# Kernel optimization log

Hardware: AMD Instinct MI355X
Metric: run time of the kernel (lower is better)

The kernel has to match this reference:

```python
import jax, jax.numpy as jnp
import numpy as np
from jax import lax

DN = ('NCHW', 'OIHW', 'NCHW')
NUM_IN_CAPS = 1152  # 32 * 6 * 6
NUM_OUT_CAPS = 10
IN_CAP_DIM = 8
OUT_CAP_DIM = 16
ROUTING_ITERS = 3


def squash(x):
    # unit_v * |x|^2 / (1 + |x|^2), norm over last dim
    n = jnp.linalg.norm(x, axis=-1, keepdims=True)
    return (x / n) * (n * n / (1.0 + n * n))


def setup_inputs() -> dict:
    key = jax.random.key(0)
    ks = jax.random.split(key, 12)
    B = 256
    return {
        'x': jax.random.normal(ks[0], (B, 1, 28, 28), jnp.float32),
        'conv1_w': jax.random.normal(ks[1], (256, 1, 9, 9), jnp.float32) * 0.05,
        'conv1_b': jnp.zeros((256,), jnp.float32),
        'pconv_w': jax.random.normal(ks[2], (256, 256, 9, 9), jnp.float32) * 0.02,
        'pconv_b': jnp.zeros((256,), jnp.float32),
        'W_caps': jax.random.normal(ks[3], (NUM_IN_CAPS, NUM_OUT_CAPS, OUT_CAP_DIM, IN_CAP_DIM), jnp.float32),
        'dec_w1': jax.random.normal(ks[4], (160, 512), jnp.float32) * 0.05,
        'dec_b1': jnp.zeros((512,), jnp.float32),
        'dec_w2': jax.random.normal(ks[5], (512, 1024), jnp.float32) * 0.04,
        'dec_b2': jnp.zeros((1024,), jnp.float32),
        'dec_w3': jax.random.normal(ks[6], (1024, 784), jnp.float32) * 0.03,
        'dec_b3': jnp.zeros((784,), jnp.float32),
    }


def reference(x, conv1_w, conv1_b, pconv_w, pconv_b, W_caps,
              dec_w1, dec_b1, dec_w2, dec_b2, dec_w3, dec_b3):
    # conv1: 1 -> 256, k9, s1, no activation (faithful to source)
    h = lax.conv_general_dilated(x, conv1_w, (1, 1), 'VALID', dimension_numbers=DN)
    h = h + conv1_b[None, :, None, None]  # (B,256,20,20)
    # primary caps conv: 256 -> 32*8, k9, s2
    h = lax.conv_general_dilated(h, pconv_w, (2, 2), 'VALID', dimension_numbers=DN)
    h = h + pconv_b[None, :, None, None]  # (B,256,6,6)
    B = h.shape[0]
    u_in = squash(h.reshape(B, -1, IN_CAP_DIM))  # (B,1152,8)
    # prediction vectors u_hat: (B,1152,10,16)
    u = jnp.einsum('ijab,nib->nija', W_caps, u_in)
    # routing-by-agreement; b is shared across batch and accumulates batch-summed agreement (faithful)
    b = jnp.zeros((NUM_IN_CAPS, NUM_OUT_CAPS), u.dtype)
    v = None
    for r in range(ROUTING_ITERS + 1):
        c = jax.nn.softmax(b, axis=-1)             # (1152,10)
        s = jnp.einsum('ij,nija->nja', c, u)        # (B,10,16)
        v = squash(s)
        if r < ROUTING_ITERS:
            b = b + jnp.einsum('nija,nja->ij', u, v)
    # decoder path: mask by predicted class
    logits = jnp.linalg.norm(v, axis=-1)            # (B,10)
    label = jnp.argmax(logits, axis=1)
    one_hot = jax.nn.one_hot(label, NUM_OUT_CAPS, dtype=v.dtype)
    recon = (one_hot[..., None] * v).reshape(B, NUM_OUT_CAPS * OUT_CAP_DIM)
    recon = jax.nn.relu(recon @ dec_w1 + dec_b1)
    recon = jax.nn.relu(recon @ dec_w2 + dec_b2)
    recon = jax.nn.sigmoid(recon @ dec_w3 + dec_b3)  # (B,784)
    return (v, recon)
```

## Files before the change

### kernel.cpp

```cpp
#include <hip/hip_runtime.h>
#include <hip/hip_fp16.h>
#include <math.h>


typedef __attribute__((ext_vector_type(8))) short short8;
typedef __attribute__((ext_vector_type(4))) float floatx4;

__device__ __forceinline__ unsigned short bf16_rne(float f) {
    unsigned int u = __float_as_uint(f);
    return (unsigned short)((u + 0x7FFFu + ((u >> 16) & 1u)) >> 16);
}
__device__ __forceinline__ float bf16_tof(unsigned short h) {
    return __uint_as_float((unsigned int)h << 16);
}
__device__ __forceinline__ void load_lds16(const void* g, void* l) {
    __builtin_amdgcn_global_load_lds(
        (const __attribute__((address_space(1))) unsigned int*)g,
        (__attribute__((address_space(3))) unsigned int*)l, 16, 0, 0);
}

__global__ __launch_bounds__(256, 2) void conv1_kernel(
    const float* __restrict__ x, const float* __restrict__ w,
    const float* __restrict__ bias, unsigned short* __restrict__ xpack)
{
    __shared__ float xs[784];
    __shared__ float wl[64 * 81];
    int t = threadIdx.x;
    int n = blockIdx.x;
    int cot = blockIdx.y;

    for (int j = t; j < 784; j += 256) xs[j] = x[n * 784 + j];
    {
        int co_s = t >> 2, k0 = (t & 3) * 21;
        const float* wsrc = w + (size_t)(cot * 64 + co_s) * 81;
        #pragma unroll
        for (int k = 0; k < 21; ++k)
            if (k0 + k < 81) wl[co_s * 81 + k0 + k] = wsrc[k0 + k];
    }
    __syncthreads();

    int co_l = t & 63, slot = t >> 6;
    int co = cot * 64 + co_l;
    float bv = bias[co];
    for (int r5 = 0; r5 < 5; ++r5) {
        int py = slot * 5 + r5;
        float acc[20];
        #pragma unroll
        for (int i = 0; i < 20; i++) acc[i] = bv;
        #pragma unroll
        for (int ky = 0; ky < 9; ++ky) {
            float xr[28];
            const float4* rowp = (const float4*)&xs[(py + ky) * 28];
            #pragma unroll
            for (int q = 0; q < 7; q++) {
                float4 v4 = rowp[q];
                xr[4*q] = v4.x; xr[4*q+1] = v4.y; xr[4*q+2] = v4.z; xr[4*q+3] = v4.w;
            }
            #pragma unroll
            for (int kx = 0; kx < 9; ++kx) {
                float wv = wl[co_l * 81 + ky * 9 + kx];
                #pragma unroll
                for (int px = 0; px < 20; ++px) acc[px] += wv * xr[px + kx];
            }
        }
        #pragma unroll
        for (int px = 0; px < 20; ++px) {
            float v = acc[px];
            unsigned short h = bf16_rne(v);
            unsigned short l = bf16_rne(v - bf16_tof(h));
            size_t pix = (size_t)n * 400 + py * 20 + px;
            xpack[pix * 512 + co] = h;
            xpack[pix * 512 + 256 + co] = l;
        }
    }
}

__global__ __launch_bounds__(256) void wpack_kernel(
    const float* __restrict__ w, unsigned short* __restrict__ wp)
{
    int tid = blockIdx.x * 256 + threadIdx.x;
    if (tid >= 648 * 16 * 64) return;
    int lane = tid & 63, g = (tid >> 6) & 15, gs = tid >> 10;
    int cb = gs & 7, kk = gs >> 3;
    int ky = kk / 9, kx = kk - ky * 9;
    int n16 = lane & 15, q = lane >> 4;
    int co = g * 16 + n16;
    unsigned short hi[8], lo[8];
    #pragma unroll
    for (int j = 0; j < 8; ++j) {
        int ci = cb * 32 + q * 8 + j;
        float v = w[((size_t)co * 256 + ci) * 81 + ky * 9 + kx];
        hi[j] = bf16_rne(v);
        lo[j] = bf16_rne(v - bf16_tof(hi[j]));
    }
    unsigned short* dst = wp + ((size_t)gs * 16 + g) * 1024 + lane * 8;
    *(short8*)dst         = *(short8*)hi;
    *(short8*)(dst + 512) = *(short8*)lo;
}

__global__ __launch_bounds__(256, 2) void pconv_mfma_kernel(
    const unsigned short* __restrict__ xp, const unsigned short* __restrict__ wp,
    __half* __restrict__ P3)
{
    __shared__ unsigned char lds[16384];
    int t = threadIdx.x;
    int lane = t & 63;
    int w = __builtin_amdgcn_readfirstlane(t >> 6);
    int mtile = blockIdx.x, kc = blockIdx.y;
    int m16 = lane & 15, q = lane >> 4;

    unsigned int asrc[2];
    #pragma unroll
    for (int j = 0; j < 2; ++j) {
        int r = w * 16 + j * 8 + (lane >> 3);
        int m = mtile * 64 + r;
        int n = m / 36, pos = m - n * 36;
        int oy = pos / 6, ox = pos - oy * 6;
        int pixbase = n * 400 + oy * 40 + ox * 2;
        int pp = (lane & 7) ^ (lane >> 3);
        int partoff = (pp < 4) ? pp * 16 : 512 + (pp - 4) * 16;
        asrc[j] = (unsigned int)(pixbase * 1024 + partoff);
    }
    const char* xb = (const char*)xp;
    const char* wb = (const char*)wp;

    floatx4 acc[4][4];
    #pragma unroll
    for (int a = 0; a < 4; ++a)
        #pragma unroll
        for (int b = 0; b < 4; ++b) acc[a][b] = (floatx4){0.f, 0.f, 0.f, 0.f};

    int slot_hi = (q ^ (m16 & 7)) * 16;
    int slot_lo = slot_hi ^ 64;

    auto stageA = [&](int s, int buf) {
        int gs = kc * 216 + s; if (gs > 647) gs = 647;
        int kk = gs >> 3, cb = gs & 7;
        int ky = kk / 9, kx = kk - ky * 9;
        unsigned int delta = (unsigned int)((ky * 20 + kx) * 1024 + cb * 64);
        #pragma unroll
        for (int j = 0; j < 2; ++j)
            load_lds16(xb + asrc[j] + delta,
                       (void*)(lds + buf * 8192 + w * 2048 + j * 1024));
    };
    auto loadB = [&](int s, short8* Bh, short8* Bl) {
        int gs = kc * 216 + s; if (gs > 647) gs = 647;
        #pragma unroll
        for (int c = 0; c < 4; ++c) {
            const char* bp = wb + ((size_t)gs * 16 + (w * 4 + c)) * 2048 + lane * 16;
            Bh[c] = *(const short8*)bp;
            Bl[c] = *(const short8*)(bp + 1024);
        }
    };
    auto compute = [&](int buf, short8* Bh, short8* Bl) {
        #pragma unroll
        for (int ms = 0; ms < 4; ++ms) {
            const char* base = (const char*)lds + buf * 8192 + (ms * 16 + m16) * 128;
            short8 Ah = *(const short8*)(base + slot_hi);
            short8 Al = *(const short8*)(base + slot_lo);
            #pragma unroll
            for (int c = 0; c < 4; ++c) {
                acc[ms][c] = __builtin_amdgcn_mfma_f32_16x16x32_bf16(Ah, Bh[c], acc[ms][c], 0, 0, 0);
                acc[ms][c] = __builtin_amdgcn_mfma_f32_16x16x32_bf16(Ah, Bl[c], acc[ms][c], 0, 0, 0);
                acc[ms][c] = __builtin_amdgcn_mfma_f32_16x16x32_bf16(Al, Bh[c], acc[ms][c], 0, 0, 0);
            }
        }
    };

    short8 Bh0[4], Bl0[4], Bh1[4], Bl1[4];
    stageA(0, 0);
    loadB(0, Bh0, Bl0);
    __syncthreads();
    for (int s = 0; s < 216; s += 2) {
        stageA(s + 1, 1);
        loadB(s + 1, Bh1, Bl1);
        compute(0, Bh0, Bl0);
        __syncthreads();
        stageA(s + 2, 0);
        loadB(s + 2, Bh0, Bl0);
        compute(1, Bh1, Bl1);
        __syncthreads();
    }

    __half* outp = P3 + ((size_t)kc * 9216 + (size_t)mtile * 64) * 256;
    #pragma unroll
    for (int ms = 0; ms < 4; ++ms)
        #pragma unroll
        for (int r = 0; r < 4; ++r) {
            int ml = ms * 16 + q * 4 + r;
            #pragma unroll
            for (int c = 0; c < 4; ++c) {
                int co = w * 64 + c * 16 + m16;
                outp[ml * 256 + co] = __float2half(acc[ms][c][r]);
            }
        }
}

__global__ __launch_bounds__(256) void squash_u_kernel(
    const __half* __restrict__ P3, const float* __restrict__ pb, float* __restrict__ u)
{
    int cap = blockIdx.x * 256 + threadIdx.x;
    int n = cap / 1152;
    int capl = cap - n * 1152;
    float z[8]; float n2 = 0.f;
    #pragma unroll
    for (int b = 0; b < 8; ++b) {
        int q2 = capl * 8 + b;
        int co = q2 / 36;
        int pos = q2 - co * 36;
        int m = n * 36 + pos;
        float s = 0.f;
        #pragma unroll
        for (int kc = 0; kc < 3; ++kc)
            s += __half2float(P3[((size_t)kc * 9216 + m) * 256 + co]);
        s += pb[co];
        z[b] = s; n2 += s * s;
    }
    float sc = sqrtf(n2) / (1.0f + n2);
    float4* op = (float4*)(u + (size_t)cap * 8);
    op[0] = make_float4(z[0]*sc, z[1]*sc, z[2]*sc, z[3]*sc);
    op[1] = make_float4(z[4]*sc, z[5]*sc, z[6]*sc, z[7]*sc);
}

__global__ void softmax_c_kernel(const float* __restrict__ b, float* __restrict__ c)
{
    int i = blockIdx.x * 256 + threadIdx.x;
    if (i >= 1152) return;
    float e[10], m = -1e30f;
    #pragma unroll
    for (int j = 0; j < 10; j++) { e[j] = b[i * 10 + j]; m = fmaxf(m, e[j]); }
    float sum = 0.f;
    #pragma unroll
    for (int j = 0; j < 10; j++) { e[j] = expf(e[j] - m); sum += e[j]; }
    float inv = 1.f / sum;
    #pragma unroll
    for (int j = 0; j < 10; j++) c[i * 10 + j] = e[j] * inv;
}

__global__ __launch_bounds__(256, 2) void s_kernel(
    const float* __restrict__ c, const float* __restrict__ u,
    const float* __restrict__ W, float* __restrict__ sbuf)
{
    int t = threadIdx.x;
    int a = t & 15, nl = t >> 4;
    int nt = blockIdx.x;
    int bz = blockIdx.y;
    int i0 = bz * 24;
    int n0 = nt * 32 + nl * 2;
    float acc[2][10];
    #pragma unroll
    for (int r = 0; r < 2; ++r)
        #pragma unroll
        for (int j = 0; j < 10; ++j) acc[r][j] = 0.f;

    for (int i = i0; i < i0 + 24; ++i) {
        const float* cb = &c[i * 10];
        float4 u0[2], u1[2];
        #pragma unroll
        for (int r = 0; r < 2; ++r) {
            const float4* up = (const float4*)&u[(size_t)(n0 + r) * 9216 + (size_t)i * 8];
            u0[r] = up[0]; u1[r] = up[1];
        }
        #pragma unroll
        for (int j = 0; j < 10; ++j) {
            const float4* wpt = (const float4*)&W[(((size_t)i * 10 + j) * 16 + a) * 8];
            float4 w0 = wpt[0], w1 = wpt[1];
            float cij = cb[j];
            #pragma unroll
            for (int r = 0; r < 2; ++r) {
                float d = w0.x*u0[r].x + w0.y*u0[r].y + w0.z*u0[r].z + w0.w*u0[r].w
                        + w1.x*u1[r].x + w1.y*u1[r].y + w1.z*u1[r].z + w1.w*u1[r].w;
                acc[r][j] += cij * d;
            }
        }
    }
    #pragma unroll
    for (int r = 0; r < 2; ++r)
        #pragma unroll
        for (int j = 0; j < 10; ++j)
            sbuf[(size_t)bz * 40960 + (((size_t)(n0 + r) * 10 + j) * 16) + a] = acc[r][j];
}

__global__ __launch_bounds__(256) void squash_v_kernel(const float* __restrict__ sbuf,
                                float* __restrict__ v, float* __restrict__ vout)
{
    int t = threadIdx.x;
    int a = t & 15;
    int idx = blockIdx.x * 16 + (t >> 4);
    float s = 0.f;
    #pragma unroll
    for (int z = 0; z < 48; ++z) s += sbuf[(size_t)z * 40960 + idx * 16 + a];
    float n2 = s * s;
    n2 += __shfl_xor(n2, 1);
    n2 += __shfl_xor(n2, 2);
    n2 += __shfl_xor(n2, 4);
    n2 += __shfl_xor(n2, 8);
    float sc = sqrtf(n2) / (1.0f + n2);
    float y = s * sc;
    v[idx * 16 + a] = y;
    if (vout) vout[idx * 16 + a] = y;
}

__global__ __launch_bounds__(192) void bupd_kernel(
    const float* __restrict__ u, const float* __restrict__ v,
    const float* __restrict__ W, float* __restrict__ b)
{
    int i0 = blockIdx.x * 4;
    int n0 = blockIdx.y * 128;
    int t = threadIdx.x;
    if (t >= 160) return;
    int j = t >> 4, a = t & 15;
    float g4[4][8];
    #pragma unroll
    for (int g = 0; g < 4; ++g)
        #pragma unroll
        for (int k = 0; k < 8; ++k) g4[g][k] = 0.f;

    for (int n = n0; n < n0 + 128; ++n) {
        float vv = v[n * 160 + t];
        const float4* ub = (const float4*)&u[(size_t)n * 9216 + (size_t)i0 * 8];
        #pragma unroll
        for (int g = 0; g < 4; ++g) {
            float4 q0 = ub[g * 2], q1 = ub[g * 2 + 1];
            g4[g][0] += q0.x * vv; g4[g][1] += q0.y * vv; g4[g][2] += q0.z * vv; g4[g][3] += q0.w * vv;
            g4[g][4] += q1.x * vv; g4[g][5] += q1.y * vv; g4[g][6] += q1.z * vv; g4[g][7] += q1.w * vv;
        }
    }
    #pragma unroll
    for (int g = 0; g < 4; ++g) {
        int i = i0 + g;
        const float4* wpt = (const float4*)&W[(((size_t)i * 10 + j) * 16 + a) * 8];
        float4 w0 = wpt[0], w1 = wpt[1];
        float p = w0.x*g4[g][0] + w0.y*g4[g][1] + w0.z*g4[g][2] + w0.w*g4[g][3]
                + w1.x*g4[g][4] + w1.y*g4[g][5] + w1.z*g4[g][6] + w1.w*g4[g][7];
        p += __shfl_xor(p, 1);
        p += __shfl_xor(p, 2);
        p += __shfl_xor(p, 4);
        p += __shfl_xor(p, 8);
        if (a == 0) atomicAdd(&b[i * 10 + j], p);
    }
}

__global__ void mask_kernel(const float* __restrict__ v, float* __restrict__ out)
{
    int n = threadIdx.x;
    const float* vp = &v[n * 160];
    int best = 0; float bestv = -1.f;
    for (int j = 0; j < 10; j++) {
        float n2 = 0.f;
        #pragma unroll
        for (int a = 0; a < 16; a++) { float y = vp[j * 16 + a]; n2 += y * y; }
        float ln = sqrtf(n2);
        if (ln > bestv) { bestv = ln; best = j; }
    }
    for (int j = 0; j < 10; j++)
        for (int a = 0; a < 16; a++)
            out[n * 160 + j * 16 + a] = (j == best) ? vp[j * 16 + a] : 0.f;
}

template<int K, int KCH, int O>
__global__ __launch_bounds__(256, 2) void mlp_part_kernel(
    const float* __restrict__ X, const float* __restrict__ Wm,
    float* __restrict__ partial)
{
    __shared__ float XS[KCH * 16];
    int t = threadIdx.x;
    int og = t & 63, ns = t >> 6;
    int n0 = blockIdx.x * 16;
    int o = blockIdx.y * 256 + og * 4;
    int o_c = min(o, O - 4);
    int ks = blockIdx.z;
    int kc0 = ks * KCH;

    for (int idx = t; idx < KCH * 16; idx += 256) {
        int k_l = idx >> 4, n_l = idx & 15;
        XS[k_l * 16 + n_l] = X[(size_t)(n0 + n_l) * K + kc0 + k_l];
    }
    __syncthreads();

    float acc[4][4];
    #pragma unroll
    for (int r = 0; r < 4; ++r)
        #pragma unroll
        for (int q = 0; q < 4; ++q) acc[r][q] = 0.f;

    #pragma unroll 8
    for (int k = 0; k < KCH; ++k) {
        float4 wv = *(const float4*)&Wm[(size_t)(kc0 + k) * O + o_c];
        float4 xs4 = *(const float4*)&XS[k * 16 + ns * 4];
        acc[0][0] += xs4.x * wv.x; acc[0][1] += xs4.x * wv.y; acc[0][2] += xs4.x * wv.z; acc[0][3] += xs4.x * wv.w;
        acc[1][0] += xs4.y * wv.x; acc[1][1] += xs4.y * wv.y; acc[1][2] += xs4.y * wv.z; acc[1][3] += xs4.y * wv.w;
        acc[2][0] += xs4.z * wv.x; acc[2][1] += xs4.z * wv.y; acc[2][2] += xs4.z * wv.z; acc[2][3] += xs4.z * wv.w;
        acc[3][0] += xs4.w * wv.x; acc[3][1] += xs4.w * wv.y; acc[3][2] += xs4.w * wv.z; acc[3][3] += xs4.w * wv.w;
    }

    if (o < O) {
        float* pp = partial + ((size_t)ks * 256 + n0 + ns * 4) * O + o;
        #pragma unroll
        for (int r = 0; r < 4; ++r)
            *(float4*)(pp + (size_t)r * O) = make_float4(acc[r][0], acc[r][1], acc[r][2], acc[r][3]);
    }
}

template<int KS, int O, int ACT>
__global__ __launch_bounds__(256) void mlp_reduce_kernel(
    const float* __restrict__ partial, const float* __restrict__ bias,
    float* __restrict__ out)
{
    int n = blockIdx.y;
    int o = (blockIdx.x * 256 + threadIdx.x) * 4;
    if (o >= O) return;
    float4 s = make_float4(0.f, 0.f, 0.f, 0.f);
    #pragma unroll
    for (int ks = 0; ks < KS; ++ks) {
        float4 p = *(const float4*)&partial[((size_t)ks * 256 + n) * O + o];
        s.x += p.x; s.y += p.y; s.z += p.z; s.w += p.w;
    }
    float4 bv = *(const float4*)&bias[o];
    float r[4] = {s.x + bv.x, s.y + bv.y, s.z + bv.z, s.w + bv.w};
    #pragma unroll
    for (int q = 0; q < 4; ++q)
        r[q] = (ACT == 0) ? fmaxf(r[q], 0.f) : (1.f / (1.f + expf(-r[q])));
    *(float4*)&out[(size_t)n * O + o] = make_float4(r[0], r[1], r[2], r[3]);
}

extern "C" void kernel_launch(void* const* d_in, const int* in_sizes, int n_in,
                              void* d_out, int out_size, void* d_ws, size_t ws_size,
                              hipStream_t stream)
{
    const float* x       = (const float*)d_in[0];
    const float* conv1_w = (const float*)d_in[1];
    const float* conv1_b = (const float*)d_in[2];
    const float* pconv_w = (const float*)d_in[3];
    const float* pconv_b = (const float*)d_in[4];
    const float* W_caps  = (const float*)d_in[5];
    const float* dec_w1  = (const float*)d_in[6];
    const float* dec_b1  = (const float*)d_in[7];
    const float* dec_w2  = (const float*)d_in[8];
    const float* dec_b2  = (const float*)d_in[9];
    const float* dec_w3  = (const float*)d_in[10];
    const float* dec_b3  = (const float*)d_in[11];
    float* out = (float*)d_out;

    float* ws = (float*)d_ws;
    size_t off = 0;
    auto alloc = [&](size_t nf) { float* p = ws + off; off += (nf + 63) & ~(size_t)63; return p; };
    unsigned short* xpack = (unsigned short*)alloc(26214400);
    unsigned short* wpack = (unsigned short*)alloc(5308416);
    __half* P3  = (__half*)alloc(3538944);
    float* u_in = alloc(2359296);
    float* bbuf = alloc(11520);
    float* cbuf = alloc(11520);
    float* sbuf = alloc(48 * 40960);
    float* vbuf = alloc(40960);
    float* rin  = alloc(40960);
    float* mpart = alloc(8 * 256 * 1024);
    float* h1   = alloc(131072);
    float* h2   = alloc(262144);

    hipMemsetAsync(bbuf, 0, 11520 * sizeof(float), stream);

    wpack_kernel<<<(648 * 16 * 64 + 255) / 256, 256, 0, stream>>>(pconv_w, wpack);
    conv1_kernel<<<dim3(256, 4), 256, 0, stream>>>(x, conv1_w, conv1_b, xpack);
    pconv_mfma_kernel<<<dim3(144, 3), 256, 0, stream>>>(xpack, wpack, P3);
    squash_u_kernel<<<1152, 256, 0, stream>>>(P3, pconv_b, u_in);

    for (int r = 0; r < 4; ++r) {
        softmax_c_kernel<<<5, 256, 0, stream>>>(bbuf, cbuf);
        s_kernel<<<dim3(8, 48), 256, 0, stream>>>(cbuf, u_in, W_caps, sbuf);
        squash_v_kernel<<<160, 256, 0, stream>>>(sbuf, vbuf, (r == 3) ? out : nullptr);
        if (r < 3) bupd_kernel<<<dim3(288, 2), 192, 0, stream>>>(u_in, vbuf, W_caps, bbuf);
    }

    mask_kernel<<<1, 256, 0, stream>>>(vbuf, rin);

    mlp_part_kernel<160, 80, 512><<<dim3(16, 2, 2), 256, 0, stream>>>(rin, dec_w1, mpart);
    mlp_reduce_kernel<2, 512, 0><<<dim3(1, 256), 256, 0, stream>>>(mpart, dec_b1, h1);
    mlp_part_kernel<512, 128, 1024><<<dim3(16, 4, 4), 256, 0, stream>>>(h1, dec_w2, mpart);
    mlp_reduce_kernel<4, 1024, 0><<<dim3(1, 256), 256, 0, stream>>>(mpart, dec_b2, h2);
    mlp_part_kernel<1024, 128, 784><<<dim3(16, 4, 8), 256, 0, stream>>>(h2, dec_w3, mpart);
    mlp_reduce_kernel<8, 784, 1><<<dim3(1, 256), 256, 0, stream>>>(mpart, dec_b3, out + 40960);
}
```

Measured before the change: 841.7 us.

## Switch pconv split-precision from bf16x3 to fp16x2, fuse softmax into s_kernel

```diff
diff --git a/kernel.cpp b/kernel.cpp
--- a/kernel.cpp
+++ b/kernel.cpp
@@ -3,15 +3,20 @@
 #include <math.h>
 
 
+typedef __attribute__((ext_vector_type(8))) _Float16 half8;
 typedef __attribute__((ext_vector_type(8))) short short8;
 typedef __attribute__((ext_vector_type(4))) float floatx4;
 
-__device__ __forceinline__ unsigned short bf16_rne(float f) {
-    unsigned int u = __float_as_uint(f);
-    return (unsigned short)((u + 0x7FFFu + ((u >> 16) & 1u)) >> 16);
-}
-__device__ __forceinline__ float bf16_tof(unsigned short h) {
-    return __uint_as_float((unsigned int)h << 16);
+__device__ __forceinline__ unsigned short f16bits(float v) {
+    _Float16 h = (_Float16)v;
+    unsigned short b;
+    __builtin_memcpy(&b, &h, 2);
+    return b;
+}
+__device__ __forceinline__ float f16back(unsigned short b) {
+    _Float16 h;
+    __builtin_memcpy(&h, &b, 2);
+    return (float)h;
 }
 __device__ __forceinline__ void load_lds16(const void* g, void* l) {
     __builtin_amdgcn_global_load_lds(
@@ -66,8 +71,8 @@
         #pragma unroll
         for (int px = 0; px < 20; ++px) {
             float v = acc[px];
-            unsigned short h = bf16_rne(v);
-            unsigned short l = bf16_rne(v - bf16_tof(h));
+            unsigned short h = f16bits(v);
+            unsigned short l = f16bits(v - f16back(h));
             size_t pix = (size_t)n * 400 + py * 20 + px;
             xpack[pix * 512 + co] = h;
             xpack[pix * 512 + 256 + co] = l;
@@ -85,24 +90,21 @@
     int ky = kk / 9, kx = kk - ky * 9;
     int n16 = lane & 15, q = lane >> 4;
     int co = g * 16 + n16;
-    unsigned short hi[8], lo[8];
+    unsigned short hv[8];
     #pragma unroll
     for (int j = 0; j < 8; ++j) {
         int ci = cb * 32 + q * 8 + j;
-        float v = w[((size_t)co * 256 + ci) * 81 + ky * 9 + kx];
-        hi[j] = bf16_rne(v);
-        lo[j] = bf16_rne(v - bf16_tof(hi[j]));
-    }
-    unsigned short* dst = wp + ((size_t)gs * 16 + g) * 1024 + lane * 8;
-    *(short8*)dst         = *(short8*)hi;
-    *(short8*)(dst + 512) = *(short8*)lo;
+        hv[j] = f16bits(w[((size_t)co * 256 + ci) * 81 + ky * 9 + kx]);
+    }
+    unsigned short* dst = wp + ((size_t)gs * 16 + g) * 512 + lane * 8;
+    *(short8*)dst = *(short8*)hv;
 }
 
 __global__ __launch_bounds__(256, 2) void pconv_mfma_kernel(
     const unsigned short* __restrict__ xp, const unsigned short* __restrict__ wp,
     __half* __restrict__ P3)
 {
-    __shared__ unsigned char lds[16384];
+    __shared__ unsigned char lds[32768];
     int t = threadIdx.x;
     int lane = t & 63;
     int w = __builtin_amdgcn_readfirstlane(t >> 6);
@@ -133,52 +135,52 @@
     int slot_hi = (q ^ (m16 & 7)) * 16;
     int slot_lo = slot_hi ^ 64;
 
-    auto stageA = [&](int s, int buf) {
-        int gs = kc * 216 + s; if (gs > 647) gs = 647;
-        int kk = gs >> 3, cb = gs & 7;
-        int ky = kk / 9, kx = kk - ky * 9;
-        unsigned int delta = (unsigned int)((ky * 20 + kx) * 1024 + cb * 64);
-        #pragma unroll
-        for (int j = 0; j < 2; ++j)
-            load_lds16(xb + asrc[j] + delta,
-                       (void*)(lds + buf * 8192 + w * 2048 + j * 1024));
+    auto stageP = [&](int p, int buf) {
+        #pragma unroll
+        for (int e = 0; e < 2; ++e) {
+            int s = 2 * p + e; if (s > 215) s = 215;
+            int gs = kc * 216 + s;
+            int kk = gs >> 3, cb = gs & 7;
+            int ky = kk / 9, kx = kk - ky * 9;
+            unsigned int delta = (unsigned int)((ky * 20 + kx) * 1024 + cb * 64);
+            #pragma unroll
+            for (int j = 0; j < 2; ++j)
+                load_lds16(xb + asrc[j] + delta,
+                           (void*)(lds + buf * 16384 + e * 8192 + w * 2048 + j * 1024));
+        }
     };
-    auto loadB = [&](int s, short8* Bh, short8* Bl) {
-        int gs = kc * 216 + s; if (gs > 647) gs = 647;
-        #pragma unroll
-        for (int c = 0; c < 4; ++c) {
-            const char* bp = wb + ((size_t)gs * 16 + (w * 4 + c)) * 2048 + lane * 16;
-            Bh[c] = *(const short8*)bp;
-            Bl[c] = *(const short8*)(bp + 1024);
-        }
+    auto loadB = [&](int s, half8* B) {
+        if (s > 215) s = 215;
+        int gs = kc * 216 + s;
+        #pragma unroll
+        for (int c = 0; c < 4; ++c)
+            B[c] = *(const half8*)(wb + ((size_t)gs * 16 + (w * 4 + c)) * 1024 + lane * 16);
     };
-    auto compute = [&](int buf, short8* Bh, short8* Bl) {
+    auto compute = [&](int buf, int e, half8* B) {
         #pragma unroll
         for (int ms = 0; ms < 4; ++ms) {
-            const char* base = (const char*)lds + buf * 8192 + (ms * 16 + m16) * 128;
-            short8 Ah = *(const short8*)(base + slot_hi);
-            short8 Al = *(const short8*)(base + slot_lo);
+            const char* base = (const char*)lds + buf * 16384 + e * 8192 + (ms * 16 + m16) * 128;
+            half8 Ah = *(const half8*)(base + slot_hi);
+            half8 Al = *(const half8*)(base + slot_lo);
             #pragma unroll
             for (int c = 0; c < 4; ++c) {
-                acc[ms][c] = __builtin_amdgcn_mfma_f32_16x16x32_bf16(Ah, Bh[c], acc[ms][c], 0, 0, 0);
-                acc[ms][c] = __builtin_amdgcn_mfma_f32_16x16x32_bf16(Ah, Bl[c], acc[ms][c], 0, 0, 0);
-                acc[ms][c] = __builtin_amdgcn_mfma_f32_16x16x32_bf16(Al, Bh[c], acc[ms][c], 0, 0, 0);
+                acc[ms][c] = __builtin_amdgcn_mfma_f32_16x16x32_f16(Ah, B[c], acc[ms][c], 0, 0, 0);
+                acc[ms][c] = __builtin_amdgcn_mfma_f32_16x16x32_f16(Al, B[c], acc[ms][c], 0, 0, 0);
             }
         }
     };
 
-    short8 Bh0[4], Bl0[4], Bh1[4], Bl1[4];
-    stageA(0, 0);
-    loadB(0, Bh0, Bl0);
+    half8 Bcur[4], Bnext[4];
+    stageP(0, 0);
+    loadB(0, Bcur);
     __syncthreads();
-    for (int s = 0; s < 216; s += 2) {
-        stageA(s + 1, 1);
-        loadB(s + 1, Bh1, Bl1);
-        compute(0, Bh0, Bl0);
-        __syncthreads();
-        stageA(s + 2, 0);
-        loadB(s + 2, Bh0, Bl0);
-        compute(1, Bh1, Bl1);
+    for (int p = 0; p < 108; ++p) {
+        int buf = p & 1;
+        stageP(p + 1, buf ^ 1);
+        loadB(2 * p + 1, Bnext);
+        compute(buf, 0, Bcur);
+        loadB(2 * p + 2, Bcur);
+        compute(buf, 1, Bnext);
         __syncthreads();
     }
 
@@ -222,31 +224,32 @@
     op[1] = make_float4(z[4]*sc, z[5]*sc, z[6]*sc, z[7]*sc);
 }
 
-__global__ void softmax_c_kernel(const float* __restrict__ b, float* __restrict__ c)
-{
-    int i = blockIdx.x * 256 + threadIdx.x;
-    if (i >= 1152) return;
-    float e[10], m = -1e30f;
-    #pragma unroll
-    for (int j = 0; j < 10; j++) { e[j] = b[i * 10 + j]; m = fmaxf(m, e[j]); }
-    float sum = 0.f;
-    #pragma unroll
-    for (int j = 0; j < 10; j++) { e[j] = expf(e[j] - m); sum += e[j]; }
-    float inv = 1.f / sum;
-    #pragma unroll
-    for (int j = 0; j < 10; j++) c[i * 10 + j] = e[j] * inv;
-}
-
 __global__ __launch_bounds__(256, 2) void s_kernel(
-    const float* __restrict__ c, const float* __restrict__ u,
+    const float* __restrict__ b, const float* __restrict__ u,
     const float* __restrict__ W, float* __restrict__ sbuf)
 {
+    __shared__ float cs[24][10];
     int t = threadIdx.x;
     int a = t & 15, nl = t >> 4;
     int nt = blockIdx.x;
     int bz = blockIdx.y;
     int i0 = bz * 24;
     int n0 = nt * 32 + nl * 2;
+
+    if (t < 24) {
+        int i = i0 + t;
+        float e[10], m = -1e30f;
+        #pragma unroll
+        for (int j = 0; j < 10; j++) { e[j] = b[i * 10 + j]; m = fmaxf(m, e[j]); }
+        float sum = 0.f;
+        #pragma unroll
+        for (int j = 0; j < 10; j++) { e[j] = expf(e[j] - m); sum += e[j]; }
+        float inv = 1.f / sum;
+        #pragma unroll
+        for (int j = 0; j < 10; j++) cs[t][j] = e[j] * inv;
+    }
+    __syncthreads();
+
     float acc[2][10];
     #pragma unroll
     for (int r = 0; r < 2; ++r)
@@ -254,7 +257,6 @@
         for (int j = 0; j < 10; ++j) acc[r][j] = 0.f;
 
     for (int i = i0; i < i0 + 24; ++i) {
-        const float* cb = &c[i * 10];
         float4 u0[2], u1[2];
         #pragma unroll
         for (int r = 0; r < 2; ++r) {
@@ -265,7 +267,7 @@
         for (int j = 0; j < 10; ++j) {
             const float4* wpt = (const float4*)&W[(((size_t)i * 10 + j) * 16 + a) * 8];
             float4 w0 = wpt[0], w1 = wpt[1];
-            float cij = cb[j];
+            float cij = cs[i - i0][j];
             #pragma unroll
             for (int r = 0; r < 2; ++r) {
                 float d = w0.x*u0[r].x + w0.y*u0[r].y + w0.z*u0[r].z + w0.w*u0[r].w
@@ -446,11 +448,10 @@
     size_t off = 0;
     auto alloc = [&](size_t nf) { float* p = ws + off; off += (nf + 63) & ~(size_t)63; return p; };
     unsigned short* xpack = (unsigned short*)alloc(26214400);
-    unsigned short* wpack = (unsigned short*)alloc(5308416);
+    unsigned short* wpack = (unsigned short*)alloc(2654208);
     __half* P3  = (__half*)alloc(3538944);
     float* u_in = alloc(2359296);
     float* bbuf = alloc(11520);
-    float* cbuf = alloc(11520);
     float* sbuf = alloc(48 * 40960);
     float* vbuf = alloc(40960);
     float* rin  = alloc(40960);
@@ -466,8 +467,7 @@
     squash_u_kernel<<<1152, 256, 0, stream>>>(P3, pconv_b, u_in);
 
     for (int r = 0; r < 4; ++r) {
-        softmax_c_kernel<<<5, 256, 0, stream>>>(bbuf, cbuf);
-        s_kernel<<<dim3(8, 48), 256, 0, stream>>>(cbuf, u_in, W_caps, sbuf);
+        s_kernel<<<dim3(8, 48), 256, 0, stream>>>(bbuf, u_in, W_caps, sbuf);
         squash_v_kernel<<<160, 256, 0, stream>>>(sbuf, vbuf, (r == 3) ? out : nullptr);
         if (r < 3) bupd_kernel<<<dim3(288, 2), 192, 0, stream>>>(u_in, vbuf, W_caps, bbuf);
     }
```

After: 763.6 us. 9.3% less time.
